# Performance work log

Hardware: AMD Instinct MI355X
Metric: run time of the kernel (lower is better)

## Reference

```python
import jax, jax.numpy as jnp
import numpy as np

NEG_SLOPE = 0.2  # PyG GATConv default leaky_relu slope
EPS = 1e-16


def gat_conv(x, src, dst, W, att_src, att_dst, bias, heads, concat):
    """PyG-style GATConv. x: [N, Fin]; W: [Fin, heads*C]; att_*: [heads, C].
    Edge (src j -> dst i): alpha_ij = softmax_i(leaky_relu(a_src.h_j + a_dst.h_i)).
    """
    N = x.shape[0]
    h = (x @ W).reshape(N, heads, -1)                       # [N, H, C]
    a_s = jnp.einsum('nhc,hc->nh', h, att_src)              # [N, H]
    a_d = jnp.einsum('nhc,hc->nh', h, att_dst)              # [N, H]
    e = jax.nn.leaky_relu(a_s[src] + a_d[dst], NEG_SLOPE)   # [E, H]
    # numerically stable segment softmax over incoming edges of each dst node
    e_max = jax.ops.segment_max(e, dst, num_segments=N)     # [N, H]
    e_max = jnp.where(jnp.isfinite(e_max), e_max, 0.0)      # isolated nodes
    ex = jnp.exp(e - e_max[dst])                            # [E, H]
    denom = jax.ops.segment_sum(ex, dst, num_segments=N)    # [N, H]
    alpha = ex / (denom[dst] + EPS)                         # [E, H]
    msg = alpha[:, :, None] * h[src]                        # [E, H, C]
    out = jax.ops.segment_sum(msg, dst, num_segments=N)     # [N, H, C]
    out = out.reshape(N, -1) if concat else out.mean(axis=1)
    return out + bias


def setup_inputs() -> dict:
    key = jax.random.key(0)
    ks = jax.random.split(key, 12)
    N, E = 100000, 1600000
    Fin, hidden, heads, Fout = 128, 128, 8, 64
    C1 = hidden // heads  # 16
    s = lambda f: 1.0 / np.sqrt(f)
    x = jax.random.normal(ks[0], (N, Fin), dtype=jnp.float32)
    edge_index = jax.random.randint(ks[1], (2, E), 0, N, dtype=jnp.int64)
    W1 = jax.random.normal(ks[2], (Fin, heads * C1), dtype=jnp.float32) * s(Fin)
    att_src1 = jax.random.normal(ks[3], (heads, C1), dtype=jnp.float32) * s(C1)
    att_dst1 = jax.random.normal(ks[4], (heads, C1), dtype=jnp.float32) * s(C1)
    b1 = jnp.zeros((hidden,), dtype=jnp.float32)
    W2 = jax.random.normal(ks[5], (hidden, Fout), dtype=jnp.float32) * s(hidden)
    att_src2 = jax.random.normal(ks[6], (1, Fout), dtype=jnp.float32) * s(Fout)
    att_dst2 = jax.random.normal(ks[7], (1, Fout), dtype=jnp.float32) * s(Fout)
    b2 = jnp.zeros((Fout,), dtype=jnp.float32)
    return {"x": x, "edge_index": edge_index,
            "W1": W1, "att_src1": att_src1, "att_dst1": att_dst1, "b1": b1,
            "W2": W2, "att_src2": att_src2, "att_dst2": att_dst2, "b2": b2}


def reference(x, edge_index, W1, att_src1, att_dst1, b1, W2, att_src2, att_dst2, b2):
    # eval mode: dropouts are identity
    src, dst = edge_index[0], edge_index[1]
    h = gat_conv(x, src, dst, W1, att_src1, att_dst1, b1, heads=8, concat=True)
    h = jax.nn.elu(h)
    out = gat_conv(h, src, dst, W2, att_src2, att_dst2, b2, heads=1, concat=False)
    return out
```

## Files before the change

### kernel.cpp

```cpp
#include <hip/hip_runtime.h>
#include <hip/hip_bf16.h>
#include <stdint.h>

#define SLOPE 0.2f
#define EPSV 1e-16f
#define H1W 72
#define H2W 36

#define NPB   512
#define NBMAX 256
#define NBLK1 256

typedef __attribute__((ext_vector_type(8))) short bf16x8;
typedef __attribute__((ext_vector_type(4))) float f32x4;

static __device__ __forceinline__ uint32_t cvtpk(float a, float b) {
    uint32_t r;
    asm("v_cvt_pk_bf16_f32 %0, %1, %2" : "=v"(r) : "v"(a), "v"(b));
    return r;
}
static __device__ __forceinline__ float lof(uint32_t u) { return __uint_as_float(u << 16); }
static __device__ __forceinline__ float hif(uint32_t u) { return __uint_as_float(u & 0xffff0000u); }

union FragCvt { uint4 u; bf16x8 f; };

__global__ __launch_bounds__(256) void prep_kernel(
    const float* __restrict__ W1, const float* __restrict__ W2,
    uint32_t* __restrict__ wt1hi, uint32_t* __restrict__ wt1lo,
    uint32_t* __restrict__ wt2hi, uint32_t* __restrict__ wt2lo)
{
    int t = threadIdx.x;
    if (blockIdx.x == 0) {
        for (int i = t; i < 128 * 64; i += 256) {
            int n = i >> 6, kp = i & 63;
            float w0 = W1[(2 * kp) * 128 + n], w1 = W1[(2 * kp + 1) * 128 + n];
            uint32_t h = cvtpk(w0, w1);
            wt1hi[n * 64 + kp] = h;
            wt1lo[n * 64 + kp] = cvtpk(w0 - lof(h), w1 - hif(h));
        }
    } else {
        for (int i = t; i < 64 * 64; i += 256) {
            int n = i >> 6, kp = i & 63;
            float w0 = W2[(2 * kp) * 64 + n], w1 = W2[(2 * kp + 1) * 64 + n];
            uint32_t h = cvtpk(w0, w1);
            wt2hi[n * 64 + kp] = h;
            wt2lo[n * 64 + kp] = cvtpk(w0 - lof(h), w1 - hif(h));
        }
    }
}

__global__ __launch_bounds__(256) void gemm1_mfma(
    const float* __restrict__ x,
    const uint32_t* __restrict__ wthi, const uint32_t* __restrict__ wtlo,
    const float* __restrict__ att_src, const float* __restrict__ att_dst,
    uint32_t* __restrict__ h1p, float* __restrict__ ad1, int N)
{
    __shared__ uint32_t lds[2][128 * 36];
    const int t = threadIdx.x;
    const int w = t >> 6, l = t & 63;
    const int cl = l & 15, rg = l >> 4;
    const int rowbase = blockIdx.x * 128 + w * 32;

    f32x4 zero = {0.f, 0.f, 0.f, 0.f};
    f32x4 acc[2][8];
    #pragma unroll
    for (int rt = 0; rt < 2; ++rt)
        #pragma unroll
        for (int tl = 0; tl < 8; ++tl) acc[rt][tl] = zero;

    for (int kh = 0; kh < 2; ++kh) {
        if (kh) __syncthreads();
        for (int i = t; i < 1024; i += 256) {
            int col = i >> 3, q = i & 7;
            *(uint4*)&lds[0][col * 36 + q * 4] = *(const uint4*)&wthi[col * 64 + kh * 32 + q * 4];
            *(uint4*)&lds[1][col * 36 + q * 4] = *(const uint4*)&wtlo[col * 64 + kh * 32 + q * 4];
        }
        __syncthreads();
        #pragma unroll
        for (int ks = 0; ks < 2; ++ks) {
            const int kg = kh * 64 + ks * 32 + rg * 8;
            bf16x8 ahi[2], alo[2];
            #pragma unroll
            for (int rt = 0; rt < 2; ++rt) {
                int row = rowbase + rt * 16 + cl;
                row = min(row, N - 1);
                const float* xr = x + (size_t)row * 128 + kg;
                float4 v0 = *(const float4*)xr;
                float4 v1 = *(const float4*)(xr + 4);
                uint32_t h0 = cvtpk(v0.x, v0.y), h1 = cvtpk(v0.z, v0.w);
                uint32_t h2 = cvtpk(v1.x, v1.y), h3 = cvtpk(v1.z, v1.w);
                uint32_t l0 = cvtpk(v0.x - lof(h0), v0.y - hif(h0));
                uint32_t l1 = cvtpk(v0.z - lof(h1), v0.w - hif(h1));
                uint32_t l2 = cvtpk(v1.x - lof(h2), v1.y - hif(h2));
                uint32_t l3 = cvtpk(v1.z - lof(h3), v1.w - hif(h3));
                FragCvt ch, clo;
                ch.u  = make_uint4(h0, h1, h2, h3);
                clo.u = make_uint4(l0, l1, l2, l3);
                ahi[rt] = ch.f; alo[rt] = clo.f;
            }
            #pragma unroll
            for (int tl = 0; tl < 8; ++tl) {
                const int off = (tl * 16 + cl) * 36 + ks * 16 + rg * 4;
                bf16x8 bhi = *(const bf16x8*)&lds[0][off];
                bf16x8 blo = *(const bf16x8*)&lds[1][off];
                #pragma unroll
                for (int rt = 0; rt < 2; ++rt) {
                    acc[rt][tl] = __builtin_amdgcn_mfma_f32_16x16x32_bf16(alo[rt], bhi, acc[rt][tl], 0, 0, 0);
                    acc[rt][tl] = __builtin_amdgcn_mfma_f32_16x16x32_bf16(ahi[rt], blo, acc[rt][tl], 0, 0, 0);
                    acc[rt][tl] = __builtin_amdgcn_mfma_f32_16x16x32_bf16(ahi[rt], bhi, acc[rt][tl], 0, 0, 0);
                }
            }
        }
    }

    #pragma unroll
    for (int rt = 0; rt < 2; ++rt) {
        const int rowb = rowbase + rt * 16 + rg * 4;
        #pragma unroll
        for (int tl = 0; tl < 8; ++tl) {
            f32x4 a = acc[rt][tl];
            float as_ = att_src[tl * 16 + cl], ad_ = att_dst[tl * 16 + cl];
            float s0 = a.x * as_, s1 = a.y * as_, s2 = a.z * as_, s3 = a.w * as_;
            float d0 = a.x * ad_, d1 = a.y * ad_, d2 = a.z * ad_, d3 = a.w * ad_;
            #pragma unroll
            for (int off = 1; off < 16; off <<= 1) {
                s0 += __shfl_xor(s0, off); s1 += __shfl_xor(s1, off);
                s2 += __shfl_xor(s2, off); s3 += __shfl_xor(s3, off);
                d0 += __shfl_xor(d0, off); d1 += __shfl_xor(d1, off);
                d2 += __shfl_xor(d2, off); d3 += __shfl_xor(d3, off);
            }
            float av[4] = {a.x, a.y, a.z, a.w};
            #pragma unroll
            for (int r = 0; r < 4; ++r) {
                float partner = __shfl_xor(av[r], 1);
                if (!(cl & 1)) {
                    int row = rowb + r;
                    if (row < N)
                        h1p[(size_t)row * H1W + tl * 8 + (cl >> 1)] = cvtpk(av[r], partner);
                }
            }
            if (cl == 0) {
                float sv[4] = {s0, s1, s2, s3}, dv[4] = {d0, d1, d2, d3};
                #pragma unroll
                for (int r = 0; r < 4; ++r) {
                    int row = rowb + r;
                    if (row < N) {
                        h1p[(size_t)row * H1W + 64 + tl] = __float_as_uint(sv[r]);
                        ad1[row * 8 + tl] = dv[r];
                    }
                }
            }
        }
    }
}

__global__ __launch_bounds__(256) void gemm2_mfma(
    const float* __restrict__ h,
    const uint32_t* __restrict__ wthi, const uint32_t* __restrict__ wtlo,
    const float* __restrict__ att_src, const float* __restrict__ att_dst,
    uint32_t* __restrict__ h2p, float* __restrict__ ad2, int N)
{
    __shared__ uint32_t lds[2][64 * 36];
    const int t = threadIdx.x;
    const int w = t >> 6, l = t & 63;
    const int cl = l & 15, rg = l >> 4;
    const int rowbase = blockIdx.x * 128 + w * 32;

    f32x4 zero = {0.f, 0.f, 0.f, 0.f};
    f32x4 acc[2][4];
    #pragma unroll
    for (int rt = 0; rt < 2; ++rt)
        #pragma unroll
        for (int tl = 0; tl < 4; ++tl) acc[rt][tl] = zero;

    for (int kh = 0; kh < 2; ++kh) {
        if (kh) __syncthreads();
        for (int i = t; i < 512; i += 256) {
            int col = i >> 3, q = i & 7;
            *(uint4*)&lds[0][col * 36 + q * 4] = *(const uint4*)&wthi[col * 64 + kh * 32 + q * 4];
            *(uint4*)&lds[1][col * 36 + q * 4] = *(const uint4*)&wtlo[col * 64 + kh * 32 + q * 4];
        }
        __syncthreads();
        #pragma unroll
        for (int ks = 0; ks < 2; ++ks) {
            const int kg = kh * 64 + ks * 32 + rg * 8;
            bf16x8 ahi[2], alo[2];
            #pragma unroll
            for (int rt = 0; rt < 2; ++rt) {
                int row = rowbase + rt * 16 + cl;
                row = min(row, N - 1);
                const float* xr = h + (size_t)row * 128 + kg;
                float4 v0 = *(const float4*)xr;
                float4 v1 = *(const float4*)(xr + 4);
                uint32_t h0 = cvtpk(v0.x, v0.y), h1 = cvtpk(v0.z, v0.w);
                uint32_t h2 = cvtpk(v1.x, v1.y), h3 = cvtpk(v1.z, v1.w);
                uint32_t l0 = cvtpk(v0.x - lof(h0), v0.y - hif(h0));
                uint32_t l1 = cvtpk(v0.z - lof(h1), v0.w - hif(h1));
                uint32_t l2 = cvtpk(v1.x - lof(h2), v1.y - hif(h2));
                uint32_t l3 = cvtpk(v1.z - lof(h3), v1.w - hif(h3));
                FragCvt ch, clo;
                ch.u  = make_uint4(h0, h1, h2, h3);
                clo.u = make_uint4(l0, l1, l2, l3);
                ahi[rt] = ch.f; alo[rt] = clo.f;
            }
            #pragma unroll
            for (int tl = 0; tl < 4; ++tl) {
                const int off = (tl * 16 + cl) * 36 + ks * 16 + rg * 4;
                bf16x8 bhi = *(const bf16x8*)&lds[0][off];
                bf16x8 blo = *(const bf16x8*)&lds[1][off];
                #pragma unroll
                for (int rt = 0; rt < 2; ++rt) {
                    acc[rt][tl] = __builtin_amdgcn_mfma_f32_16x16x32_bf16(alo[rt], bhi, acc[rt][tl], 0, 0, 0);
                    acc[rt][tl] = __builtin_amdgcn_mfma_f32_16x16x32_bf16(ahi[rt], blo, acc[rt][tl], 0, 0, 0);
                    acc[rt][tl] = __builtin_amdgcn_mfma_f32_16x16x32_bf16(ahi[rt], bhi, acc[rt][tl], 0, 0, 0);
                }
            }
        }
    }

    #pragma unroll
    for (int rt = 0; rt < 2; ++rt) {
        const int rowb = rowbase + rt * 16 + rg * 4;
        float s0 = 0.f, s1 = 0.f, s2 = 0.f, s3 = 0.f;
        float d0 = 0.f, d1 = 0.f, d2 = 0.f, d3 = 0.f;
        #pragma unroll
        for (int tl = 0; tl < 4; ++tl) {
            f32x4 a = acc[rt][tl];
            float as_ = att_src[tl * 16 + cl], ad_ = att_dst[tl * 16 + cl];
            s0 += a.x * as_; s1 += a.y * as_; s2 += a.z * as_; s3 += a.w * as_;
            d0 += a.x * ad_; d1 += a.y * ad_; d2 += a.z * ad_; d3 += a.w * ad_;
            float av[4] = {a.x, a.y, a.z, a.w};
            #pragma unroll
            for (int r = 0; r < 4; ++r) {
                float partner = __shfl_xor(av[r], 1);
                if (!(cl & 1)) {
                    int row = rowb + r;
                    if (row < N)
                        h2p[(size_t)row * H2W + tl * 8 + (cl >> 1)] = cvtpk(av[r], partner);
                }
            }
        }
        #pragma unroll
        for (int off = 1; off < 16; off <<= 1) {
            s0 += __shfl_xor(s0, off); s1 += __shfl_xor(s1, off);
            s2 += __shfl_xor(s2, off); s3 += __shfl_xor(s3, off);
            d0 += __shfl_xor(d0, off); d1 += __shfl_xor(d1, off);
            d2 += __shfl_xor(d2, off); d3 += __shfl_xor(d3, off);
        }
        if (cl == 0) {
            float sv[4] = {s0, s1, s2, s3}, dv[4] = {d0, d1, d2, d3};
            #pragma unroll
            for (int r = 0; r < 4; ++r) {
                int row = rowb + r;
                if (row < N) {
                    h2p[(size_t)row * H2W + 32] = __float_as_uint(sv[r]);
                    ad2[row] = dv[r];
                }
            }
        }
    }
}

__global__ __launch_bounds__(256) void p1_count_kernel(
    const int* __restrict__ ei, int* __restrict__ pbh, int E, int NB, int chunk)
{
    __shared__ int hist[NBMAX];
    int t = threadIdx.x;
    if (t < NB) hist[t] = 0;
    __syncthreads();
    int e0 = blockIdx.x * chunk;
    int e1 = min(E, e0 + chunk);
    for (int e = e0 + t; e < e1; e += 256)
        atomicAdd(&hist[ei[E + e] >> 9], 1);
    __syncthreads();
    if (t < NB) pbh[t * NBLK1 + blockIdx.x] = hist[t];
}

__global__ __launch_bounds__(256) void p1_scan_kernel(
    int* __restrict__ pbh, int* __restrict__ bucket_base, int NB, int E)
{
    __shared__ int ps[256];
    int t = threadIdx.x;
    int s = 0;
    if (t < NB) {
        const int* row = &pbh[t * NBLK1];
        for (int b = 0; b < NBLK1; ++b) s += row[b];
    }
    ps[t] = s; __syncthreads();
    for (int off = 1; off < 256; off <<= 1) {
        int add = (t >= off) ? ps[t - off] : 0;
        __syncthreads();
        ps[t] += add;
        __syncthreads();
    }
    int base = ps[t] - s;
    if (t < NB) {
        bucket_base[t] = base;
        int* row = &pbh[t * NBLK1];
        int run = base;
        for (int b = 0; b < NBLK1; ++b) {
            int c = row[b];
            row[b] = run;
            run += c;
        }
    }
    if (t == 0) bucket_base[NB] = E;
}

__global__ __launch_bounds__(256) void p1_place_kernel(
    const int* __restrict__ ei, const int* __restrict__ pbh,
    uint32_t* __restrict__ staging, int E, int NB, int chunk)
{
    __shared__ int lcur[NBMAX];
    int t = threadIdx.x;
    if (t < NB) lcur[t] = pbh[t * NBLK1 + blockIdx.x];
    __syncthreads();
    int e0 = blockIdx.x * chunk;
    int e1 = min(E, e0 + chunk);
    for (int e = e0 + t; e < e1; e += 256) {
        int s = ei[e], d = ei[E + e];
        int b = d >> 9;
        int p = atomicAdd(&lcur[b], 1);
        staging[p] = ((uint32_t)s << 9) | (uint32_t)(d & 511);
    }
}

__global__ __launch_bounds__(256) void p2_build_kernel(
    const uint32_t* __restrict__ staging, const int* __restrict__ bucket_base,
    int* __restrict__ row_start, int* __restrict__ sorted_src, int N, int E, int NB)
{
    __shared__ int cnt[NPB];
    __shared__ int ofs[NPB];
    __shared__ int ps[256];
    int b = blockIdx.x, t = threadIdx.x;
    int base = bucket_base[b], end = bucket_base[b + 1];
    cnt[t] = 0; cnt[t + 256] = 0;
    __syncthreads();
    for (int i = base + t; i < end; i += 256)
        atomicAdd(&cnt[staging[i] & 511], 1);
    __syncthreads();
    int c0 = cnt[2 * t], c1 = cnt[2 * t + 1];
    int p = c0 + c1;
    ps[t] = p; __syncthreads();
    for (int off = 1; off < 256; off <<= 1) {
        int add = (t >= off) ? ps[t - off] : 0;
        __syncthreads();
        ps[t] += add;
        __syncthreads();
    }
    int pex = ps[t] - p;
    ofs[2 * t] = pex;
    ofs[2 * t + 1] = pex + c0;
    __syncthreads();
    int node0 = b * NPB;
    #pragma unroll
    for (int i = t; i < NPB; i += 256) {
        int node = node0 + i;
        if (node < N) row_start[node] = base + ofs[i];
    }
    if (b == NB - 1 && t == 0) row_start[N] = E;
    __syncthreads();
    for (int i = base + t; i < end; i += 256) {
        uint32_t v = staging[i];
        int nl = v & 511;
        int pos = base + atomicAdd(&ofs[nl], 1);
        sorted_src[pos] = (int)(v >> 9);
    }
}

__global__ __launch_bounds__(256) void gather1_kernel(
    const int* __restrict__ row_start, const int* __restrict__ sorted_src,
    const float* __restrict__ ad1, const uint32_t* __restrict__ h1p,
    const float* __restrict__ b1, float* __restrict__ hbuf, int N)
{
    int node = blockIdx.x * 4 + (threadIdx.x >> 6);
    if (node >= N) return;
    const int l   = threadIdx.x & 63;
    const int wh  = l & 7;
    const int eA  = l >> 3;
    const int c4  = l & 31;
    const int par = l >> 5;
    const int hB  = c4 >> 2;

    int r0 = row_start[node], r1 = row_start[node + 1];

    if (r0 == r1) {
        if (l < 32) {
            float4 bv = *(const float4*)&b1[c4 * 4];
            bv.x = bv.x > 0.f ? bv.x : expm1f(bv.x);
            bv.y = bv.y > 0.f ? bv.y : expm1f(bv.y);
            bv.z = bv.z > 0.f ? bv.z : expm1f(bv.z);
            bv.w = bv.w > 0.f ? bv.w : expm1f(bv.w);
            *(float4*)&hbuf[(size_t)node * 128 + c4 * 4] = bv;
        }
        return;
    }

    float adw = ad1[node * 8 + wh];
    float acc0 = 0.f, acc1 = 0.f, acc2 = 0.f, acc3 = 0.f, den = 0.f;

    int jw = r0 + eA;
    int sw0 = sorted_src[jw < r1 ? jw : r0] * H1W;
    int j1 = r0 + 8 + eA;
    int sw1 = sorted_src[j1 < r1 ? j1 : r0] * H1W;
    float av0 = __uint_as_float(h1p[sw0 + 64 + wh]);

    for (int j = r0; j < r1; j += 8) {
        int jn = j + 16 + eA;
        int swn = sorted_src[jn < r1 ? jn : r0] * H1W;
        float avn = __uint_as_float(h1p[sw1 + 64 + wh]);

        float ev = av0 + adw;
        ev = ev > 0.f ? ev : SLOPE * ev;
        float w = (j + eA) < r1 ? __expf(ev) : 0.f;
        den += w;

        #pragma unroll
        for (int k = 0; k < 4; ++k) {
            int eidx = 2 * k + par;
            float wk  = __shfl(w,   eidx * 8 + hB, 64);
            int   ofk = __shfl(sw0, eidx * 8,      64);
            uint2 hv = *(const uint2*)&h1p[ofk + 2 * c4];
            acc0 = fmaf(wk, lof(hv.x), acc0);
            acc1 = fmaf(wk, hif(hv.x), acc1);
            acc2 = fmaf(wk, lof(hv.y), acc2);
            acc3 = fmaf(wk, hif(hv.y), acc3);
        }
        sw0 = sw1; sw1 = swn; av0 = avn;
    }

    den += __shfl_xor(den, 8, 64);
    den += __shfl_xor(den, 16, 64);
    den += __shfl_xor(den, 32, 64);
    float dB = __shfl(den, hB, 64);

    acc0 += __shfl_xor(acc0, 32, 64);
    acc1 += __shfl_xor(acc1, 32, 64);
    acc2 += __shfl_xor(acc2, 32, 64);
    acc3 += __shfl_xor(acc3, 32, 64);

    if (l < 32) {
        float inv = 1.0f / (dB + EPSV);
        float4 bv = *(const float4*)&b1[c4 * 4];
        float v0 = acc0 * inv + bv.x;
        float v1 = acc1 * inv + bv.y;
        float v2 = acc2 * inv + bv.z;
        float v3 = acc3 * inv + bv.w;
        v0 = v0 > 0.f ? v0 : expm1f(v0);
        v1 = v1 > 0.f ? v1 : expm1f(v1);
        v2 = v2 > 0.f ? v2 : expm1f(v2);
        v3 = v3 > 0.f ? v3 : expm1f(v3);
        *(float4*)&hbuf[(size_t)node * 128 + c4 * 4] = make_float4(v0, v1, v2, v3);
    }
}

__global__ __launch_bounds__(256) void gather2_kernel(
    const int* __restrict__ row_start, const int* __restrict__ sorted_src,
    const float* __restrict__ ad2, const uint32_t* __restrict__ h2p,
    const float* __restrict__ b2, float* __restrict__ out, int N)
{
    int node = blockIdx.x * 8 + (threadIdx.x >> 5);
    if (node >= N) return;
    const int l   = threadIdx.x & 31;
    const int eA  = l & 7;
    const int c4  = l & 15;
    const int par = (l >> 4) & 1;

    int r0 = row_start[node], r1 = row_start[node + 1];

    if (r0 == r1) {
        if (l < 16) {
            float4 bv = *(const float4*)&b2[c4 * 4];
            *(float4*)&out[(size_t)node * 64 + c4 * 4] = bv;
        }
        return;
    }

    float ad = ad2[node];
    float acc0 = 0.f, acc1 = 0.f, acc2 = 0.f, acc3 = 0.f, den = 0.f;

    int jw = r0 + eA;
    int sw0 = sorted_src[jw < r1 ? jw : r0] * H2W;
    int j1 = r0 + 8 + eA;
    int sw1 = sorted_src[j1 < r1 ? j1 : r0] * H2W;
    float av0 = __uint_as_float(h2p[sw0 + 32]);

    for (int j = r0; j < r1; j += 8) {
        int jn = j + 16 + eA;
        int swn = sorted_src[jn < r1 ? jn : r0] * H2W;
        float avn = __uint_as_float(h2p[sw1 + 32]);

        float ev = av0 + ad;
        ev = ev > 0.f ? ev : SLOPE * ev;
        float w = (j + eA) < r1 ? __expf(ev) : 0.f;
        den += w;

        #pragma unroll
        for (int k = 0; k < 4; ++k) {
            int eidx = 2 * k + par;
            float wk  = __shfl(w,   eidx, 32);
            int   ofk = __shfl(sw0, eidx, 32);
            uint2 hv = *(const uint2*)&h2p[ofk + 2 * c4];
            acc0 = fmaf(wk, lof(hv.x), acc0);
            acc1 = fmaf(wk, hif(hv.x), acc1);
            acc2 = fmaf(wk, lof(hv.y), acc2);
            acc3 = fmaf(wk, hif(hv.y), acc3);
        }
        sw0 = sw1; sw1 = swn; av0 = avn;
    }

    den += __shfl_xor(den, 1, 32);
    den += __shfl_xor(den, 2, 32);
    den += __shfl_xor(den, 4, 32);
    acc0 += __shfl_xor(acc0, 16, 32);
    acc1 += __shfl_xor(acc1, 16, 32);
    acc2 += __shfl_xor(acc2, 16, 32);
    acc3 += __shfl_xor(acc3, 16, 32);

    if (l < 16) {
        float inv = 1.0f / (den + EPSV);
        float4 bv = *(const float4*)&b2[c4 * 4];
        *(float4*)&out[(size_t)node * 64 + c4 * 4] =
            make_float4(acc0 * inv + bv.x, acc1 * inv + bv.y,
                        acc2 * inv + bv.z, acc3 * inv + bv.w);
    }
}

extern "C" void kernel_launch(void* const* d_in, const int* in_sizes, int n_in,
                              void* d_out, int out_size, void* d_ws, size_t ws_size,
                              hipStream_t stream)
{
    const int N = in_sizes[0] / 128;
    const int E = in_sizes[1] / 2;
    const int NB = (N + NPB - 1) / NPB;
    const int chunk = (E + NBLK1 - 1) / NBLK1;

    const float* x        = (const float*)d_in[0];
    const int*   ei       = (const int*)  d_in[1];
    const float* W1       = (const float*)d_in[2];
    const float* att_src1 = (const float*)d_in[3];
    const float* att_dst1 = (const float*)d_in[4];
    const float* b1       = (const float*)d_in[5];
    const float* W2       = (const float*)d_in[6];
    const float* att_src2 = (const float*)d_in[7];
    const float* att_dst2 = (const float*)d_in[8];
    const float* b2       = (const float*)d_in[9];
    float* out = (float*)d_out;

    uint32_t* h1p  = (uint32_t*)d_ws;
    float* hbuf    = (float*)(h1p + (size_t)N * H1W);
    float* ad1     = hbuf + (size_t)N * 128;
    float* ad2     = ad1  + (size_t)N * 8;
    int* row_start   = (int*)(ad2 + N);
    int* bucket_base = row_start + (N + 1);
    int* pbh         = bucket_base + (NB + 1);
    int* sorted_src  = pbh + NB * NBLK1;
    uint32_t* staging = (uint32_t*)(sorted_src + E);
    uint32_t* wt1hi = staging + E;
    uint32_t* wt1lo = wt1hi + 128 * 64;
    uint32_t* wt2hi = wt1lo + 128 * 64;
    uint32_t* wt2lo = wt2hi + 64 * 64;
    uint32_t* h2p   = h1p;

    prep_kernel<<<2, 256, 0, stream>>>(W1, W2, wt1hi, wt1lo, wt2hi, wt2lo);

    p1_count_kernel<<<NBLK1, 256, 0, stream>>>(ei, pbh, E, NB, chunk);
    p1_scan_kernel <<<1, 256, 0, stream>>>(pbh, bucket_base, NB, E);
    p1_place_kernel<<<NBLK1, 256, 0, stream>>>(ei, pbh, staging, E, NB, chunk);
    p2_build_kernel<<<NB, 256, 0, stream>>>(staging, bucket_base, row_start, sorted_src, N, E, NB);

    gemm1_mfma<<<(N + 127) / 128, 256, 0, stream>>>(x, wt1hi, wt1lo, att_src1, att_dst1, h1p, ad1, N);
    gather1_kernel<<<(N + 3) / 4, 256, 0, stream>>>(row_start, sorted_src, ad1, h1p, b1, hbuf, N);

    gemm2_mfma<<<(N + 127) / 128, 256, 0, stream>>>(hbuf, wt2hi, wt2lo, att_src2, att_dst2, h2p, ad2, N);
    gather2_kernel<<<(N + 7) / 8, 256, 0, stream>>>(row_start, sorted_src, ad2, h2p, b2, out, N);
}
```

Baseline: 280.1 us.

## Store features as fp16, gather with 16-byte loads, fold log2e into attention

The packed node features move from bf16 to fp16 via cvt_pkrtz. Both gather kernels are restructured so each lane loads 8 halves (uint4) per edge instead of 4 bf16 (uint2), processing 4 edges per pass with a two-step cross-lane reduction. The attention vectors are pre-scaled by log2(e) so the edge weight uses exp2f instead of __expf. The aim is fewer, wider memory transactions in the gather and slightly cheaper exponentials. The trade-off is fp16 range limits on the stored features and more shuffle reductions at the end.

Measured after the change: 283.4 us. No clear change (+1.2%).

```diff
diff --git a/kernel.cpp b/kernel.cpp
--- a/kernel.cpp
+++ b/kernel.cpp
@@ -1,9 +1,11 @@
 #include <hip/hip_runtime.h>
 #include <hip/hip_bf16.h>
+#include <hip/hip_fp16.h>
 #include <stdint.h>
 
 #define SLOPE 0.2f
 #define EPSV 1e-16f
+#define LOG2E 1.44269504f
 #define H1W 72
 #define H2W 36
 
@@ -21,6 +23,12 @@
 }
 static __device__ __forceinline__ float lof(uint32_t u) { return __uint_as_float(u << 16); }
 static __device__ __forceinline__ float hif(uint32_t u) { return __uint_as_float(u & 0xffff0000u); }
+
+static __device__ __forceinline__ uint32_t pkf16(float a, float b) {
+    auto r = __builtin_amdgcn_cvt_pkrtz(a, b);
+    return __builtin_bit_cast(uint32_t, r);
+}
+union F16W { uint32_t u; _Float16 h[2]; };
 
 union FragCvt { uint4 u; bf16x8 f; };
 
@@ -119,7 +127,7 @@
         #pragma unroll
         for (int tl = 0; tl < 8; ++tl) {
             f32x4 a = acc[rt][tl];
-            float as_ = att_src[tl * 16 + cl], ad_ = att_dst[tl * 16 + cl];
+            float as_ = att_src[tl * 16 + cl] * LOG2E, ad_ = att_dst[tl * 16 + cl] * LOG2E;
             float s0 = a.x * as_, s1 = a.y * as_, s2 = a.z * as_, s3 = a.w * as_;
             float d0 = a.x * ad_, d1 = a.y * ad_, d2 = a.z * ad_, d3 = a.w * ad_;
             #pragma unroll
@@ -136,7 +144,7 @@
                 if (!(cl & 1)) {
                     int row = rowb + r;
                     if (row < N)
-                        h1p[(size_t)row * H1W + tl * 8 + (cl >> 1)] = cvtpk(av[r], partner);
+                        h1p[(size_t)row * H1W + tl * 8 + (cl >> 1)] = pkf16(av[r], partner);
                 }
             }
             if (cl == 0) {
@@ -226,7 +234,7 @@
         #pragma unroll
         for (int tl = 0; tl < 4; ++tl) {
             f32x4 a = acc[rt][tl];
-            float as_ = att_src[tl * 16 + cl], ad_ = att_dst[tl * 16 + cl];
+            float as_ = att_src[tl * 16 + cl] * LOG2E, ad_ = att_dst[tl * 16 + cl] * LOG2E;
             s0 += a.x * as_; s1 += a.y * as_; s2 += a.z * as_; s3 += a.w * as_;
             d0 += a.x * ad_; d1 += a.y * ad_; d2 += a.z * ad_; d3 += a.w * ad_;
             float av[4] = {a.x, a.y, a.z, a.w};
@@ -236,7 +244,7 @@
                 if (!(cl & 1)) {
                     int row = rowb + r;
                     if (row < N)
-                        h2p[(size_t)row * H2W + tl * 8 + (cl >> 1)] = cvtpk(av[r], partner);
+                        h2p[(size_t)row * H2W + tl * 8 + (cl >> 1)] = pkf16(av[r], partner);
                 }
             }
         }
@@ -375,29 +383,34 @@
 {
     int node = blockIdx.x * 4 + (threadIdx.x >> 6);
     if (node >= N) return;
-    const int l   = threadIdx.x & 63;
-    const int wh  = l & 7;
-    const int eA  = l >> 3;
-    const int c4  = l & 31;
-    const int par = l >> 5;
-    const int hB  = c4 >> 2;
+    const int l  = threadIdx.x & 63;
+    const int wh = l & 7;
+    const int eA = l >> 3;
+    const int c8 = l & 15;
+    const int q  = l >> 4;
+    const int hB = c8 >> 1;
 
     int r0 = row_start[node], r1 = row_start[node + 1];
 
     if (r0 == r1) {
-        if (l < 32) {
-            float4 bv = *(const float4*)&b1[c4 * 4];
-            bv.x = bv.x > 0.f ? bv.x : expm1f(bv.x);
-            bv.y = bv.y > 0.f ? bv.y : expm1f(bv.y);
-            bv.z = bv.z > 0.f ? bv.z : expm1f(bv.z);
-            bv.w = bv.w > 0.f ? bv.w : expm1f(bv.w);
-            *(float4*)&hbuf[(size_t)node * 128 + c4 * 4] = bv;
+        if (l < 16) {
+            #pragma unroll
+            for (int g = 0; g < 2; ++g) {
+                float4 bv = *(const float4*)&b1[c8 * 8 + g * 4];
+                bv.x = bv.x > 0.f ? bv.x : expm1f(bv.x);
+                bv.y = bv.y > 0.f ? bv.y : expm1f(bv.y);
+                bv.z = bv.z > 0.f ? bv.z : expm1f(bv.z);
+                bv.w = bv.w > 0.f ? bv.w : expm1f(bv.w);
+                *(float4*)&hbuf[(size_t)node * 128 + c8 * 8 + g * 4] = bv;
+            }
         }
         return;
     }
 
     float adw = ad1[node * 8 + wh];
-    float acc0 = 0.f, acc1 = 0.f, acc2 = 0.f, acc3 = 0.f, den = 0.f;
+    const uint32_t* rowp = h1p + 4 * c8;
+    float acc[8] = {0.f, 0.f, 0.f, 0.f, 0.f, 0.f, 0.f, 0.f};
+    float den = 0.f;
 
     int jw = r0 + eA;
     int sw0 = sorted_src[jw < r1 ? jw : r0] * H1W;
@@ -412,19 +425,25 @@
 
         float ev = av0 + adw;
         ev = ev > 0.f ? ev : SLOPE * ev;
-        float w = (j + eA) < r1 ? __expf(ev) : 0.f;
+        float w = (j + eA) < r1 ? exp2f(ev) : 0.f;
         den += w;
 
         #pragma unroll
-        for (int k = 0; k < 4; ++k) {
-            int eidx = 2 * k + par;
+        for (int k = 0; k < 2; ++k) {
+            int eidx = q + 4 * k;
             float wk  = __shfl(w,   eidx * 8 + hB, 64);
             int   ofk = __shfl(sw0, eidx * 8,      64);
-            uint2 hv = *(const uint2*)&h1p[ofk + 2 * c4];
-            acc0 = fmaf(wk, lof(hv.x), acc0);
-            acc1 = fmaf(wk, hif(hv.x), acc1);
-            acc2 = fmaf(wk, lof(hv.y), acc2);
-            acc3 = fmaf(wk, hif(hv.y), acc3);
+            uint4 hv = *(const uint4*)(rowp + ofk);
+            F16W u0, u1, u2, u3;
+            u0.u = hv.x; u1.u = hv.y; u2.u = hv.z; u3.u = hv.w;
+            acc[0] = fmaf((float)u0.h[0], wk, acc[0]);
+            acc[1] = fmaf((float)u0.h[1], wk, acc[1]);
+            acc[2] = fmaf((float)u1.h[0], wk, acc[2]);
+            acc[3] = fmaf((float)u1.h[1], wk, acc[3]);
+            acc[4] = fmaf((float)u2.h[0], wk, acc[4]);
+            acc[5] = fmaf((float)u2.h[1], wk, acc[5]);
+            acc[6] = fmaf((float)u3.h[0], wk, acc[6]);
+            acc[7] = fmaf((float)u3.h[1], wk, acc[7]);
         }
         sw0 = sw1; sw1 = swn; av0 = avn;
     }
@@ -434,23 +453,27 @@
     den += __shfl_xor(den, 32, 64);
     float dB = __shfl(den, hB, 64);
 
-    acc0 += __shfl_xor(acc0, 32, 64);
-    acc1 += __shfl_xor(acc1, 32, 64);
-    acc2 += __shfl_xor(acc2, 32, 64);
-    acc3 += __shfl_xor(acc3, 32, 64);
-
-    if (l < 32) {
+    #pragma unroll
+    for (int i = 0; i < 8; ++i) {
+        acc[i] += __shfl_xor(acc[i], 16, 64);
+        acc[i] += __shfl_xor(acc[i], 32, 64);
+    }
+
+    if (l < 16) {
         float inv = 1.0f / (dB + EPSV);
-        float4 bv = *(const float4*)&b1[c4 * 4];
-        float v0 = acc0 * inv + bv.x;
-        float v1 = acc1 * inv + bv.y;
-        float v2 = acc2 * inv + bv.z;
-        float v3 = acc3 * inv + bv.w;
-        v0 = v0 > 0.f ? v0 : expm1f(v0);
-        v1 = v1 > 0.f ? v1 : expm1f(v1);
-        v2 = v2 > 0.f ? v2 : expm1f(v2);
-        v3 = v3 > 0.f ? v3 : expm1f(v3);
-        *(float4*)&hbuf[(size_t)node * 128 + c4 * 4] = make_float4(v0, v1, v2, v3);
+        #pragma unroll
+        for (int g = 0; g < 2; ++g) {
+            float4 bv = *(const float4*)&b1[c8 * 8 + g * 4];
+            float v0 = acc[g * 4 + 0] * inv + bv.x;
+            float v1 = acc[g * 4 + 1] * inv + bv.y;
+            float v2 = acc[g * 4 + 2] * inv + bv.z;
+            float v3 = acc[g * 4 + 3] * inv + bv.w;
+            v0 = v0 > 0.f ? v0 : expm1f(v0);
+            v1 = v1 > 0.f ? v1 : expm1f(v1);
+            v2 = v2 > 0.f ? v2 : expm1f(v2);
+            v3 = v3 > 0.f ? v3 : expm1f(v3);
+            *(float4*)&hbuf[(size_t)node * 128 + c8 * 8 + g * 4] = make_float4(v0, v1, v2, v3);
+        }
     }
 }
 
@@ -461,23 +484,28 @@
 {
     int node = blockIdx.x * 8 + (threadIdx.x >> 5);
     if (node >= N) return;
-    const int l   = threadIdx.x & 31;
-    const int eA  = l & 7;
-    const int c4  = l & 15;
-    const int par = (l >> 4) & 1;
+    const int l  = threadIdx.x & 31;
+    const int eA = l & 7;
+    const int c8 = l & 7;
+    const int q  = l >> 3;
 
     int r0 = row_start[node], r1 = row_start[node + 1];
 
     if (r0 == r1) {
-        if (l < 16) {
-            float4 bv = *(const float4*)&b2[c4 * 4];
-            *(float4*)&out[(size_t)node * 64 + c4 * 4] = bv;
+        if (l < 8) {
+            #pragma unroll
+            for (int g = 0; g < 2; ++g) {
+                float4 bv = *(const float4*)&b2[c8 * 8 + g * 4];
+                *(float4*)&out[(size_t)node * 64 + c8 * 8 + g * 4] = bv;
+            }
         }
         return;
     }
 
     float ad = ad2[node];
-    float acc0 = 0.f, acc1 = 0.f, acc2 = 0.f, acc3 = 0.f, den = 0.f;
+    const uint32_t* rowp = h2p + 4 * c8;
+    float acc[8] = {0.f, 0.f, 0.f, 0.f, 0.f, 0.f, 0.f, 0.f};
+    float den = 0.f;
 
     int jw = r0 + eA;
     int sw0 = sorted_src[jw < r1 ? jw : r0] * H2W;
@@ -492,19 +520,25 @@
 
         float ev = av0 + ad;
         ev = ev > 0.f ? ev : SLOPE * ev;
-        float w = (j + eA) < r1 ? __expf(ev) : 0.f;
+        float w = (j + eA) < r1 ? exp2f(ev) : 0.f;
         den += w;
 
         #pragma unroll
-        for (int k = 0; k < 4; ++k) {
-            int eidx = 2 * k + par;
+        for (int k = 0; k < 2; ++k) {
+            int eidx = q + 4 * k;
             float wk  = __shfl(w,   eidx, 32);
             int   ofk = __shfl(sw0, eidx, 32);
-            uint2 hv = *(const uint2*)&h2p[ofk + 2 * c4];
-            acc0 = fmaf(wk, lof(hv.x), acc0);
-            acc1 = fmaf(wk, hif(hv.x), acc1);
-            acc2 = fmaf(wk, lof(hv.y), acc2);
-            acc3 = fmaf(wk, hif(hv.y), acc3);
+            uint4 hv = *(const uint4*)(rowp + ofk);
+            F16W u0, u1, u2, u3;
+            u0.u = hv.x; u1.u = hv.y; u2.u = hv.z; u3.u = hv.w;
+            acc[0] = fmaf((float)u0.h[0], wk, acc[0]);
+            acc[1] = fmaf((float)u0.h[1], wk, acc[1]);
+            acc[2] = fmaf((float)u1.h[0], wk, acc[2]);
+            acc[3] = fmaf((float)u1.h[1], wk, acc[3]);
+            acc[4] = fmaf((float)u2.h[0], wk, acc[4]);
+            acc[5] = fmaf((float)u2.h[1], wk, acc[5]);
+            acc[6] = fmaf((float)u3.h[0], wk, acc[6]);
+            acc[7] = fmaf((float)u3.h[1], wk, acc[7]);
         }
         sw0 = sw1; sw1 = swn; av0 = avn;
     }
@@ -512,17 +546,21 @@
     den += __shfl_xor(den, 1, 32);
     den += __shfl_xor(den, 2, 32);
     den += __shfl_xor(den, 4, 32);
-    acc0 += __shfl_xor(acc0, 16, 32);
-    acc1 += __shfl_xor(acc1, 16, 32);
-    acc2 += __shfl_xor(acc2, 16, 32);
-    acc3 += __shfl_xor(acc3, 16, 32);
-
-    if (l < 16) {
+    #pragma unroll
+    for (int i = 0; i < 8; ++i) {
+        acc[i] += __shfl_xor(acc[i], 8, 32);
+        acc[i] += __shfl_xor(acc[i], 16, 32);
+    }
+
+    if (l < 8) {
         float inv = 1.0f / (den + EPSV);
-        float4 bv = *(const float4*)&b2[c4 * 4];
-        *(float4*)&out[(size_t)node * 64 + c4 * 4] =
-            make_float4(acc0 * inv + bv.x, acc1 * inv + bv.y,
-                        acc2 * inv + bv.z, acc3 * inv + bv.w);
+        #pragma unroll
+        for (int g = 0; g < 2; ++g) {
+            float4 bv = *(const float4*)&b2[c8 * 8 + g * 4];
+            *(float4*)&out[(size_t)node * 64 + c8 * 8 + g * 4] =
+                make_float4(acc[g * 4 + 0] * inv + bv.x, acc[g * 4 + 1] * inv + bv.y,
+                            acc[g * 4 + 2] * inv + bv.z, acc[g * 4 + 3] * inv + bv.w);
+        }
     }
 }
 
```
